# Kernel tuning notes

Hardware: AMD Instinct MI355X
Metric: run time of the kernel (lower is better)

The kernel has to match this reference:

```python
import jax, jax.numpy as jnp
import numpy as np


def setup_inputs() -> dict:
    key = jax.random.key(0)
    kx, km = jax.random.split(key)
    B, D, O = 16384, 256, 32
    x = jax.random.normal(kx, (B, D), dtype=jnp.float32)
    M = jax.random.uniform(km, (D, O), dtype=jnp.float32)
    return {"x": x, "M": M}


def reference(x, M):
    # NMU forward: y[b, o] = prod_d (M_hat[d, o] * x[b, d] + 1 - M_hat[d, o])
    M_hat = jnp.clip(M, 0.0, 1.0)                      # [D, O]
    # affine broadcast: [B, D, 1] * [1, D, O] -> [B, D, O]
    t = x[:, :, None] * M_hat[None, :, :] + (1.0 - M_hat)[None, :, :]
    return jnp.prod(t, axis=1)                          # [B, O]
```

## Files before the change

### kernel.cpp

```cpp
#include <hip/hip_runtime.h>
#include <stdint.h>


typedef float v2f __attribute__((ext_vector_type(2)));

constexpr int D = 256;
constexpr int O = 32;
constexpr int ROWS_PB = 16;

template <int CTRL>
__device__ __forceinline__ float dppmul(float v) {
    int i = __builtin_bit_cast(int, v);
    int p = __builtin_amdgcn_update_dpp(i, i, CTRL, 0xF, 0xF, false);
    return v * __builtin_bit_cast(float, p);
}
template <int CTRL>
__device__ __forceinline__ v2f dppmul2(v2f v) {
    v2f r; r.x = dppmul<CTRL>(v.x); r.y = dppmul<CTRL>(v.y); return r;
}
__device__ __forceinline__ v2f clamp01(v2f v) {
    v = __builtin_elementwise_max(v, (v2f)0.0f);
    return __builtin_elementwise_min(v, (v2f)1.0f);
}
#define TERM(mm, e) __builtin_elementwise_fma((mm), (v2f){(e), (e)}, (v2f){1.0f, 1.0f})

__global__ __launch_bounds__(256, 4)
void nmu_fwd(const float* __restrict__ x, const float* __restrict__ M,
             float* __restrict__ y)
{
    __shared__ __align__(16) float xt[ROWS_PB * D];
    __shared__ __align__(16) float part[ROWS_PB * 4 * O];
    const int tid  = threadIdx.x;
    const int lane = tid & 63;
    const int w    = tid >> 6;
    const int ds   = lane & 7;
    const int oq   = lane >> 3;
    const int row0 = blockIdx.x * ROWS_PB;

    const float4* xg = reinterpret_cast<const float4*>(x + row0 * D);
    float4 s0 = xg[tid], s1 = xg[256 + tid], s2 = xg[512 + tid], s3 = xg[768 + tid];

    const float2* M2 = reinterpret_cast<const float2*>(M);
    const int mb = (w * 64 + ds * 8) * (O / 2) + oq * 2;
#define MLOAD(dd) \
    float2 l##dd = M2[mb + (dd) * 16]; float2 h##dd = M2[mb + (dd) * 16 + 1]; \
    v2f mL##dd = clamp01((v2f){l##dd.x, l##dd.y});                            \
    v2f mH##dd = clamp01((v2f){h##dd.x, h##dd.y});
    MLOAD(0) MLOAD(1) MLOAD(2) MLOAD(3) MLOAD(4) MLOAD(5) MLOAD(6) MLOAD(7)
#undef MLOAD

    float4* lp = reinterpret_cast<float4*>(xt);
    lp[tid] = s0; lp[256 + tid] = s1; lp[512 + tid] = s2; lp[768 + tid] = s3;
    __syncthreads();

    const int xoff = w * 16 + ds * 2;
    const float4* lt = reinterpret_cast<const float4*>(xt);
#pragma unroll 1
    for (int r = 0; r < ROWS_PB; ++r) {
        const float4 xa = lt[r * 64 + xoff];
        const float4 xb = lt[r * 64 + xoff + 1];
        const float e0 = xa.x - 1.0f, e1 = xa.y - 1.0f;
        const float e2 = xa.z - 1.0f, e3 = xa.w - 1.0f;
        const float e4 = xb.x - 1.0f, e5 = xb.y - 1.0f;
        const float e6 = xb.z - 1.0f, e7 = xb.w - 1.0f;

        v2f pL = (TERM(mL0, e0) * TERM(mL1, e1)) * (TERM(mL2, e2) * TERM(mL3, e3));
        pL    *= (TERM(mL4, e4) * TERM(mL5, e5)) * (TERM(mL6, e6) * TERM(mL7, e7));
        v2f pH = (TERM(mH0, e0) * TERM(mH1, e1)) * (TERM(mH2, e2) * TERM(mH3, e3));
        pH    *= (TERM(mH4, e4) * TERM(mH5, e5)) * (TERM(mH6, e6) * TERM(mH7, e7));

        pL = dppmul2<0xB1>(pL); pL = dppmul2<0x4E>(pL); pL = dppmul2<0x141>(pL);
        pH = dppmul2<0xB1>(pH); pH = dppmul2<0x4E>(pH); pH = dppmul2<0x141>(pH);

        if (ds == 0) {
            float4 pv = {pL.x, pL.y, pH.x, pH.y};
            *reinterpret_cast<float4*>(&part[(r * 4 + w) * O + oq * 4]) = pv;
        }
    }
    __syncthreads();

    {
        const int mr = tid >> 4;
        const int op = tid & 15;
        const v2f* pp = reinterpret_cast<const v2f*>(part);
        v2f a = pp[(mr * 4 + 0) * (O / 2) + op] * pp[(mr * 4 + 1) * (O / 2) + op];
        v2f b = pp[(mr * 4 + 2) * (O / 2) + op] * pp[(mr * 4 + 3) * (O / 2) + op];
        a *= b;
        *reinterpret_cast<v2f*>(y + (row0 + mr) * O + op * 2) = a;
    }
}

extern "C" void kernel_launch(void* const* d_in, const int* in_sizes, int n_in,
                              void* d_out, int out_size, void* d_ws, size_t ws_size,
                              hipStream_t stream) {
    const float* x = (const float*)d_in[0];
    const float* M = (const float*)d_in[1];
    float* y = (float*)d_out;
    const int B = in_sizes[0] / D;
    dim3 grid(B / ROWS_PB);
    nmu_fwd<<<grid, 256, 0, stream>>>(x, M, y);
}
```

Before: 73.35 us.

## Remove LDS staging; each wave reduces full D for half of O and streams x

Each wave now handles 8 rows and 16 outputs over the full D=256, with 16 lanes each covering 16 d values. This replaces the LDS staging of x and the cross-wave partial-product reduction in shared memory with an extra DPP step and direct global stores. x rows are prefetched one row ahead straight from global memory into registers. Register pressure goes up (32 v2f M values per lane), and each x row is now read by two waves instead of once per block.

Result: slower. 79.04 us (+7.8%).

```diff
diff --git a/kernel.cpp b/kernel.cpp
--- a/kernel.cpp
+++ b/kernel.cpp
@@ -6,7 +6,7 @@
 
 constexpr int D = 256;
 constexpr int O = 32;
-constexpr int ROWS_PB = 16;
+constexpr int WROWS = 8;
 
 template <int CTRL>
 __device__ __forceinline__ float dppmul(float v) {
@@ -28,65 +28,65 @@
 void nmu_fwd(const float* __restrict__ x, const float* __restrict__ M,
              float* __restrict__ y)
 {
-    __shared__ __align__(16) float xt[ROWS_PB * D];
-    __shared__ __align__(16) float part[ROWS_PB * 4 * O];
     const int tid  = threadIdx.x;
     const int lane = tid & 63;
-    const int w    = tid >> 6;
-    const int ds   = lane & 7;
-    const int oq   = lane >> 3;
-    const int row0 = blockIdx.x * ROWS_PB;
+    const int wv   = tid >> 6;
+    const int ds   = lane & 15;
+    const int oq   = lane >> 4;
+    const int h    = wv & 1;
+    const int rg   = wv >> 1;
+    const int row0 = blockIdx.x * (2 * WROWS) + rg * WROWS;
+    const int o0   = h * 16 + oq * 4;
 
-    const float4* xg = reinterpret_cast<const float4*>(x + row0 * D);
-    float4 s0 = xg[tid], s1 = xg[256 + tid], s2 = xg[512 + tid], s3 = xg[768 + tid];
-
-    const float2* M2 = reinterpret_cast<const float2*>(M);
-    const int mb = (w * 64 + ds * 8) * (O / 2) + oq * 2;
+    const float4* M4 = reinterpret_cast<const float4*>(M);
+    const int mb = ds * 16 * (O / 4) + (o0 >> 2);
 #define MLOAD(dd) \
-    float2 l##dd = M2[mb + (dd) * 16]; float2 h##dd = M2[mb + (dd) * 16 + 1]; \
-    v2f mL##dd = clamp01((v2f){l##dd.x, l##dd.y});                            \
-    v2f mH##dd = clamp01((v2f){h##dd.x, h##dd.y});
-    MLOAD(0) MLOAD(1) MLOAD(2) MLOAD(3) MLOAD(4) MLOAD(5) MLOAD(6) MLOAD(7)
+    float4 mv##dd = M4[mb + (dd) * (O / 4)];                      \
+    v2f mL##dd = clamp01((v2f){mv##dd.x, mv##dd.y});              \
+    v2f mH##dd = clamp01((v2f){mv##dd.z, mv##dd.w});
+    MLOAD(0)  MLOAD(1)  MLOAD(2)  MLOAD(3)
+    MLOAD(4)  MLOAD(5)  MLOAD(6)  MLOAD(7)
+    MLOAD(8)  MLOAD(9)  MLOAD(10) MLOAD(11)
+    MLOAD(12) MLOAD(13) MLOAD(14) MLOAD(15)
 #undef MLOAD
 
-    float4* lp = reinterpret_cast<float4*>(xt);
-    lp[tid] = s0; lp[256 + tid] = s1; lp[512 + tid] = s2; lp[768 + tid] = s3;
-    __syncthreads();
+    const float4* xbase = reinterpret_cast<const float4*>(x + (size_t)row0 * D) + ds * 4;
+    constexpr int RS4 = D / 4;
 
-    const int xoff = w * 16 + ds * 2;
-    const float4* lt = reinterpret_cast<const float4*>(xt);
+    float4 a0 = xbase[0], a1 = xbase[1], a2 = xbase[2], a3 = xbase[3];
+
 #pragma unroll 1
-    for (int r = 0; r < ROWS_PB; ++r) {
-        const float4 xa = lt[r * 64 + xoff];
-        const float4 xb = lt[r * 64 + xoff + 1];
-        const float e0 = xa.x - 1.0f, e1 = xa.y - 1.0f;
-        const float e2 = xa.z - 1.0f, e3 = xa.w - 1.0f;
-        const float e4 = xb.x - 1.0f, e5 = xb.y - 1.0f;
-        const float e6 = xb.z - 1.0f, e7 = xb.w - 1.0f;
+    for (int r = 0; r < WROWS; ++r) {
+        const int rn = (r + 1) & (WROWS - 1);
+        const float4* xn = xbase + rn * RS4;
+        float4 b0 = xn[0], b1 = xn[1], b2 = xn[2], b3 = xn[3];
 
-        v2f pL = (TERM(mL0, e0) * TERM(mL1, e1)) * (TERM(mL2, e2) * TERM(mL3, e3));
-        pL    *= (TERM(mL4, e4) * TERM(mL5, e5)) * (TERM(mL6, e6) * TERM(mL7, e7));
-        v2f pH = (TERM(mH0, e0) * TERM(mH1, e1)) * (TERM(mH2, e2) * TERM(mH3, e3));
-        pH    *= (TERM(mH4, e4) * TERM(mH5, e5)) * (TERM(mH6, e6) * TERM(mH7, e7));
+        const float e0  = a0.x - 1.0f, e1  = a0.y - 1.0f, e2  = a0.z - 1.0f, e3  = a0.w - 1.0f;
+        const float e4  = a1.x - 1.0f, e5  = a1.y - 1.0f, e6  = a1.z - 1.0f, e7  = a1.w - 1.0f;
+        const float e8  = a2.x - 1.0f, e9  = a2.y - 1.0f, e10 = a2.z - 1.0f, e11 = a2.w - 1.0f;
+        const float e12 = a3.x - 1.0f, e13 = a3.y - 1.0f, e14 = a3.z - 1.0f, e15 = a3.w - 1.0f;
 
-        pL = dppmul2<0xB1>(pL); pL = dppmul2<0x4E>(pL); pL = dppmul2<0x141>(pL);
-        pH = dppmul2<0xB1>(pH); pH = dppmul2<0x4E>(pH); pH = dppmul2<0x141>(pH);
+        v2f pL = (TERM(mL0,  e0)  * TERM(mL1,  e1))  * (TERM(mL2,  e2)  * TERM(mL3,  e3));
+        pL    *= (TERM(mL4,  e4)  * TERM(mL5,  e5))  * (TERM(mL6,  e6)  * TERM(mL7,  e7));
+        pL    *= (TERM(mL8,  e8)  * TERM(mL9,  e9))  * (TERM(mL10, e10) * TERM(mL11, e11));
+        pL    *= (TERM(mL12, e12) * TERM(mL13, e13)) * (TERM(mL14, e14) * TERM(mL15, e15));
+
+        v2f pH = (TERM(mH0,  e0)  * TERM(mH1,  e1))  * (TERM(mH2,  e2)  * TERM(mH3,  e3));
+        pH    *= (TERM(mH4,  e4)  * TERM(mH5,  e5))  * (TERM(mH6,  e6)  * TERM(mH7,  e7));
+        pH    *= (TERM(mH8,  e8)  * TERM(mH9,  e9))  * (TERM(mH10, e10) * TERM(mH11, e11));
+        pH    *= (TERM(mH12, e12) * TERM(mH13, e13)) * (TERM(mH14, e14) * TERM(mH15, e15));
+
+        pL = dppmul2<0xB1>(pL);  pH = dppmul2<0xB1>(pH);
+        pL = dppmul2<0x4E>(pL);  pH = dppmul2<0x4E>(pH);
+        pL = dppmul2<0x141>(pL); pH = dppmul2<0x141>(pH);
+        pL = dppmul2<0x140>(pL); pH = dppmul2<0x140>(pH);
 
         if (ds == 0) {
-            float4 pv = {pL.x, pL.y, pH.x, pH.y};
-            *reinterpret_cast<float4*>(&part[(r * 4 + w) * O + oq * 4]) = pv;
+            float4 out = {pL.x, pL.y, pH.x, pH.y};
+            *reinterpret_cast<float4*>(y + (size_t)(row0 + r) * O + o0) = out;
         }
-    }
-    __syncthreads();
 
-    {
-        const int mr = tid >> 4;
-        const int op = tid & 15;
-        const v2f* pp = reinterpret_cast<const v2f*>(part);
-        v2f a = pp[(mr * 4 + 0) * (O / 2) + op] * pp[(mr * 4 + 1) * (O / 2) + op];
-        v2f b = pp[(mr * 4 + 2) * (O / 2) + op] * pp[(mr * 4 + 3) * (O / 2) + op];
-        a *= b;
-        *reinterpret_cast<v2f*>(y + (row0 + mr) * O + op * 2) = a;
+        a0 = b0; a1 = b1; a2 = b2; a3 = b3;
     }
 }
 
@@ -97,6 +97,6 @@
     const float* M = (const float*)d_in[1];
     float* y = (float*)d_out;
     const int B = in_sizes[0] / D;
-    dim3 grid(B / ROWS_PB);
+    dim3 grid(B / (2 * WROWS));
     nmu_fwd<<<grid, 256, 0, stream>>>(x, M, y);
 }
```

## Precompute 1-M terms, prefetch next x row, and shorten DPP reduction

Applied to the files above, without the earlier changes.

Each term becomes fma(m, x, 1-m) with 1-M_hat precomputed in registers, which removes the eight per-row subtractions x-1. The LDS loads for the next row are issued one iteration ahead so their latency overlaps the current row's math. The cross-lane reduction stops after two DPP steps, and two lanes per group write partial products into a doubled shared buffer, leaving a wider 8-way product for the final stage. The cost is extra registers for the complement values and prefetched data, plus more shared memory and LDS traffic in the epilogue.

New measurement: 72.79 us. About the same (-0.8%).

```diff
diff --git a/kernel.cpp b/kernel.cpp
--- a/kernel.cpp
+++ b/kernel.cpp
@@ -22,14 +22,14 @@
     v = __builtin_elementwise_max(v, (v2f)0.0f);
     return __builtin_elementwise_min(v, (v2f)1.0f);
 }
-#define TERM(mm, e) __builtin_elementwise_fma((mm), (v2f){(e), (e)}, (v2f){1.0f, 1.0f})
+#define T(mm, cc, xx) __builtin_elementwise_fma((mm), (v2f){(xx), (xx)}, (cc))
 
 __global__ __launch_bounds__(256, 4)
 void nmu_fwd(const float* __restrict__ x, const float* __restrict__ M,
              float* __restrict__ y)
 {
     __shared__ __align__(16) float xt[ROWS_PB * D];
-    __shared__ __align__(16) float part[ROWS_PB * 4 * O];
+    __shared__ __align__(16) float part[ROWS_PB * 8 * O];
     const int tid  = threadIdx.x;
     const int lane = tid & 63;
     const int w    = tid >> 6;
@@ -45,7 +45,9 @@
 #define MLOAD(dd) \
     float2 l##dd = M2[mb + (dd) * 16]; float2 h##dd = M2[mb + (dd) * 16 + 1]; \
     v2f mL##dd = clamp01((v2f){l##dd.x, l##dd.y});                            \
-    v2f mH##dd = clamp01((v2f){h##dd.x, h##dd.y});
+    v2f mH##dd = clamp01((v2f){h##dd.x, h##dd.y});                            \
+    v2f cL##dd = (v2f){1.0f, 1.0f} - mL##dd;                                  \
+    v2f cH##dd = (v2f){1.0f, 1.0f} - mH##dd;
     MLOAD(0) MLOAD(1) MLOAD(2) MLOAD(3) MLOAD(4) MLOAD(5) MLOAD(6) MLOAD(7)
 #undef MLOAD
 
@@ -55,27 +57,27 @@
 
     const int xoff = w * 16 + ds * 2;
     const float4* lt = reinterpret_cast<const float4*>(xt);
+    float4 xa = lt[xoff], xb = lt[xoff + 1];
 #pragma unroll 1
     for (int r = 0; r < ROWS_PB; ++r) {
-        const float4 xa = lt[r * 64 + xoff];
-        const float4 xb = lt[r * 64 + xoff + 1];
-        const float e0 = xa.x - 1.0f, e1 = xa.y - 1.0f;
-        const float e2 = xa.z - 1.0f, e3 = xa.w - 1.0f;
-        const float e4 = xb.x - 1.0f, e5 = xb.y - 1.0f;
-        const float e6 = xb.z - 1.0f, e7 = xb.w - 1.0f;
+        const int rn = (r + 1) & (ROWS_PB - 1);
+        float4 na = lt[rn * 64 + xoff];
+        float4 nb = lt[rn * 64 + xoff + 1];
 
-        v2f pL = (TERM(mL0, e0) * TERM(mL1, e1)) * (TERM(mL2, e2) * TERM(mL3, e3));
-        pL    *= (TERM(mL4, e4) * TERM(mL5, e5)) * (TERM(mL6, e6) * TERM(mL7, e7));
-        v2f pH = (TERM(mH0, e0) * TERM(mH1, e1)) * (TERM(mH2, e2) * TERM(mH3, e3));
-        pH    *= (TERM(mH4, e4) * TERM(mH5, e5)) * (TERM(mH6, e6) * TERM(mH7, e7));
+        v2f pL = (T(mL0, cL0, xa.x) * T(mL1, cL1, xa.y)) * (T(mL2, cL2, xa.z) * T(mL3, cL3, xa.w));
+        pL    *= (T(mL4, cL4, xb.x) * T(mL5, cL5, xb.y)) * (T(mL6, cL6, xb.z) * T(mL7, cL7, xb.w));
+        v2f pH = (T(mH0, cH0, xa.x) * T(mH1, cH1, xa.y)) * (T(mH2, cH2, xa.z) * T(mH3, cH3, xa.w));
+        pH    *= (T(mH4, cH4, xb.x) * T(mH5, cH5, xb.y)) * (T(mH6, cH6, xb.z) * T(mH7, cH7, xb.w));
 
-        pL = dppmul2<0xB1>(pL); pL = dppmul2<0x4E>(pL); pL = dppmul2<0x141>(pL);
-        pH = dppmul2<0xB1>(pH); pH = dppmul2<0x4E>(pH); pH = dppmul2<0x141>(pH);
+        pL = dppmul2<0xB1>(pL); pL = dppmul2<0x4E>(pL);
+        pH = dppmul2<0xB1>(pH); pH = dppmul2<0x4E>(pH);
 
-        if (ds == 0) {
+        if ((ds & 3) == 0) {
+            const int sub = ds >> 2;
             float4 pv = {pL.x, pL.y, pH.x, pH.y};
-            *reinterpret_cast<float4*>(&part[(r * 4 + w) * O + oq * 4]) = pv;
+            *reinterpret_cast<float4*>(&part[((r * 4 + w) * 2 + sub) * O + oq * 4]) = pv;
         }
+        xa = na; xb = nb;
     }
     __syncthreads();
 
@@ -83,9 +85,12 @@
         const int mr = tid >> 4;
         const int op = tid & 15;
         const v2f* pp = reinterpret_cast<const v2f*>(part);
-        v2f a = pp[(mr * 4 + 0) * (O / 2) + op] * pp[(mr * 4 + 1) * (O / 2) + op];
-        v2f b = pp[(mr * 4 + 2) * (O / 2) + op] * pp[(mr * 4 + 3) * (O / 2) + op];
-        a *= b;
+        const int base = mr * 8 * (O / 2) + op;
+        v2f a = pp[base +  0] * pp[base + 16];
+        v2f b = pp[base + 32] * pp[base + 48];
+        v2f c = pp[base + 64] * pp[base + 80];
+        v2f d = pp[base + 96] * pp[base + 112];
+        a = (a * b) * (c * d);
         *reinterpret_cast<v2f*>(y + (row0 + mr) * O + op * 2) = a;
     }
 }
```
